# Performance work log

Hardware: AMD Instinct MI355X
Metric: run time of the kernel (lower is better)

The kernel has to match this reference:

```python
import jax, jax.numpy as jnp
import numpy as np

EPS = 1e-6
SIGMA = 1.0       # get_matrix default sigma
INIT_SIGMA = 1.0  # args.init_sigma


def setup_inputs() -> dict:
    key = jax.random.key(0)
    ks = jax.random.split(key, 12)
    B, T, LD, NB = 16, 2048, 256, 32
    s = 1.0 / np.sqrt(LD)
    E_raw = jax.random.normal(ks[5], (LD, LD), jnp.float32)
    E_w, _ = jnp.linalg.qr(E_raw)  # orthogonal like geotorch.orthogonal
    return {
        "Z": jax.random.normal(ks[0], (B, T, LD), jnp.float32),
        "obs_times": jax.random.uniform(ks[1], (B, T, 1), jnp.float32),
        "D": jax.random.normal(ks[2], (NB, LD), jnp.float32),
        "coeff_W": jax.random.normal(ks[3], (NB, LD), jnp.float32) * s,
        "coeff_b": jnp.zeros((NB,), jnp.float32),
        "E_w": E_w.astype(jnp.float32),
        "B_w": jax.random.normal(ks[6], (LD, LD), jnp.float32) * s,
        "C_w": jax.random.normal(ks[7], (LD, LD), jnp.float32) * s,
        "M_w": jax.random.normal(ks[8], (LD, LD), jnp.float32) * s,
        "init_mean_p": jax.random.normal(ks[9], (LD,), jnp.float32),
        "init_log_var": jax.random.normal(ks[10], (LD,), jnp.float32),
        "y_log_var": jax.random.normal(ks[11], (LD,), jnp.float32),
    }


def _binop(qi, qj):
    # (A_j*A_i, Bu_j + A_j*Bu_i): combine earlier element qi with later qj
    A_i, Bu_i = qi
    A_j, Bu_j = qj
    return (A_j * A_i, Bu_j + A_j * Bu_i)


def reference(Z, obs_times, D, coeff_W, coeff_b, E_w, B_w, C_w, M_w,
              init_mean_p, init_log_var, y_log_var):
    LD = Z.shape[-1]
    # alphas = B(Z)
    alphas = jnp.einsum('btd,ed->bte', Z, B_w)                      # (B,T,LD)
    # get_matrix (vectorized over batch and time)
    A_basis = -(jnp.exp(D) + EPS)                                   # (NB,LD), negative
    A_coeff = jax.nn.softmax(jnp.einsum('btd,nd->btn', alphas, coeff_W) + coeff_b, axis=-1)
    A_mat = jnp.einsum('btn,nd->btd', A_coeff, A_basis)             # (B,T,LD)
    exp_A_m = jnp.exp(A_mat * obs_times)                            # mean transition
    exp_B_m = (exp_A_m - 1.0) / A_mat * alphas
    exp_A_v = jnp.exp(2.0 * A_mat * obs_times)                      # var transition
    exp_B_v = 0.5 * SIGMA ** 2 * (exp_A_v - 1.0) / A_mat + EPS
    mats_A = jnp.concatenate([exp_A_m, exp_A_v], axis=-1)           # (B,T,2LD)
    mats_B = jnp.concatenate([exp_B_m, exp_B_v], axis=-1)           # (B,T,2LD)
    # parallel linear-recurrence scan over time
    cum_A, cum_B = jax.lax.associative_scan(_binop, (mats_A, mats_B), axis=1)
    # initial condition in rotated coordinates
    init_mean0 = E_w.T @ init_mean_p                                # (LD,)
    diag_v = INIT_SIGMA * (jnp.exp(init_log_var) + EPS)
    init_var0 = jnp.einsum('ki,k->i', E_w ** 2, diag_v)             # diag(E^T diag(v) E)
    init_mv = jnp.concatenate([init_mean0, init_var0], axis=0)      # (2LD,)
    imv = cum_A * init_mv                                           # (B,T,2LD)
    init_mean, init_var = imv[..., :LD], imv[..., LD:]
    xs_mean, xs_var = cum_B[..., :LD], cum_B[..., LD:]
    y_var = jnp.exp(y_log_var) + EPS
    # output projections: M(E(.)) and history C(E(Z))
    history = jnp.einsum('btd,ed,fe->btf', Z, E_w, C_w)
    means = jnp.einsum('btd,ed,fe->btf', xs_mean + init_mean, E_w, M_w) + history
    stds = jnp.einsum('btd,ed,fe->btf', jnp.sqrt(xs_var + init_var + y_var), E_w, M_w)
    return means, stds, alphas
```

## Files before the change

kernel.cpp:

```cpp
#include <hip/hip_runtime.h>
#include <math.h>

#define EPS 1e-6f

#define B_   16
#define T_   2048
#define LD   256
#define NB   32
#define BT   (B_ * T_)
#define NCH  64
#define CHUNK (T_ / NCH)

typedef short bf16x8 __attribute__((ext_vector_type(8)));
typedef float f32x4  __attribute__((ext_vector_type(4)));

__device__ __forceinline__ unsigned short f2b(float f) {
    unsigned int u = __float_as_uint(f);
    unsigned int r = (u + 0x7fffu + ((u >> 16) & 1u)) >> 16;
    return (unsigned short)r;
}

__device__ __forceinline__ void gl_lds16(const void* g, void* l) {
    __builtin_amdgcn_global_load_lds(
        (const __attribute__((address_space(1))) unsigned int*)g,
        (__attribute__((address_space(3))) unsigned int*)l, 16, 0, 0);
}

__device__ __forceinline__ void stage_tile(const unsigned short* __restrict__ src,
                                           int row0, int stride, int kb,
                                           unsigned short* lds, int wv, int lane) {
#pragma unroll
    for (int cc = 0; cc < 2; ++cc) {
        int c = wv * 2 + cc;
        int r = c * 16 + (lane >> 2);
        int qd = (lane & 3) ^ ((r >> 1) & 3);
        const unsigned short* g = src + (size_t)(row0 + r) * stride + kb + qd * 8;
        gl_lds16(g, lds + c * 512);
    }
}

__device__ __forceinline__ void stage_tile256(const unsigned short* __restrict__ src,
                                              int kb, unsigned short* lds, int wv, int lane) {
#pragma unroll
    for (int cc = 0; cc < 4; ++cc) {
        int c = wv * 4 + cc;
        int r = c * 16 + (lane >> 2);
        int qd = (lane & 3) ^ ((r >> 1) & 3);
        const unsigned short* g = src + (size_t)r * LD + kb + qd * 8;
        gl_lds16(g, lds + c * 512);
    }
}

__device__ __forceinline__ bf16x8 frag_ld(const unsigned short* lds, int row, int qd) {
    int pq = qd ^ ((row >> 1) & 3);
    return *(const bf16x8*)(lds + row * 32 + pq * 8);
}

__global__ __launch_bounds__(256) void k_pre(const float* __restrict__ Z,
                                             const float* __restrict__ Dm,
                                             const float* __restrict__ cw,
                                             const float* __restrict__ Ew,
                                             const float* __restrict__ Bw,
                                             const float* __restrict__ Cw,
                                             const float* __restrict__ Mw,
                                             const float* __restrict__ imp,
                                             const float* __restrict__ ilv,
                                             const float* __restrict__ ylv,
                                             unsigned short* __restrict__ GMh,
                                             unsigned short* __restrict__ GCh,
                                             unsigned short* __restrict__ cwbh,
                                             float* __restrict__ im0,
                                             float* __restrict__ iv0,
                                             float* __restrict__ yv,
                                             float* __restrict__ Ab,
                                             unsigned short* __restrict__ Bwh,
                                             unsigned short* __restrict__ Zh) {
    int bid = blockIdx.x;
    int tid = threadIdx.x;
    if (bid < 544) {
        const float* W; const float* E; unsigned short* out; int d0, f0;
        if (bid < 256)      { W = Mw; E = Ew; out = GMh;  d0 = (bid & 15) * 16; f0 = (bid >> 4) * 16; }
        else if (bid < 512) { W = Cw; E = Ew; out = GCh;  d0 = (bid & 15) * 16; f0 = ((bid - 256) >> 4) * 16; }
        else                { W = cw; E = Bw; out = cwbh; d0 = (bid & 15) * 16; f0 = ((bid - 512) >> 4) * 16; }
        __shared__ float Ws[16][17];
        __shared__ float Es[16][17];
        int tx = tid & 15, ty = tid >> 4;
        float acc = 0.f;
        for (int eb = 0; eb < LD; eb += 16) {
            Ws[ty][tx] = W[(f0 + ty) * LD + eb + tx];
            Es[ty][tx] = E[(eb + ty) * LD + d0 + tx];
            __syncthreads();
#pragma unroll
            for (int k = 0; k < 16; ++k) acc = fmaf(Ws[ty][k], Es[k][tx], acc);
            __syncthreads();
        }
        out[(f0 + ty) * LD + d0 + tx] = f2b(acc);
    } else if (bid < 577) {
        int sub = bid - 544;
        int t = tid;
        if (sub == 0) {
            float sm = 0.f, sv = 0.f;
            for (int k = 0; k < LD; ++k) {
                float e = Ew[k * LD + t];
                sm = fmaf(e, imp[k], sm);
                sv = fmaf(e * e, expf(ilv[k]) + EPS, sv);
            }
            im0[t] = sm;
            iv0[t] = sv;
            yv[t]  = expf(ylv[t]) + EPS;
        } else {
            int n = sub - 1;
            Ab[n * LD + t] = -(expf(Dm[n * LD + t]) + EPS);
        }
    } else if (bid < 641) {
        int i = (bid - 577) * 256 + tid;
        float4 v = ((const float4*)Bw)[i];
        ((ushort4*)Bwh)[i] = make_ushort4(f2b(v.x), f2b(v.y), f2b(v.z), f2b(v.w));
    } else {
        int i = (bid - 641) * 256 + tid;
        float4 v = ((const float4*)Z)[i];
        ((ushort4*)Zh)[i] = make_ushort4(f2b(v.x), f2b(v.y), f2b(v.z), f2b(v.w));
    }
}

__global__ __launch_bounds__(256) void k_zb(const unsigned short* __restrict__ Zh,
                                            const unsigned short* __restrict__ Bwh,
                                            const unsigned short* __restrict__ cwbh,
                                            const float* __restrict__ cb,
                                            float* __restrict__ alphas,
                                            float* __restrict__ logits) {
    __shared__ unsigned short As[128 * 32];
    __shared__ unsigned short Bs[128 * 32];
    int tid = threadIdx.x, lane = tid & 63, wv = tid >> 6;
    int m0 = blockIdx.x * 128;
    int y  = blockIdx.y;
    if (y < 2) {
        int n0 = y * 128;
        int wm = (wv & 1) * 64, wn = (wv >> 1) * 64;
        f32x4 acc[4][4];
#pragma unroll
        for (int i = 0; i < 4; ++i)
#pragma unroll
            for (int j = 0; j < 4; ++j) acc[i][j] = (f32x4){0.f, 0.f, 0.f, 0.f};
        for (int kb = 0; kb < LD; kb += 32) {
            stage_tile(Zh, m0, LD, kb, As, wv, lane);
            stage_tile(Bwh, n0, LD, kb, Bs, wv, lane);
            __syncthreads();
            int qd = lane >> 4;
            bf16x8 af[4], bf[4];
#pragma unroll
            for (int i = 0; i < 4; ++i) af[i] = frag_ld(As, wm + i * 16 + (lane & 15), qd);
#pragma unroll
            for (int j = 0; j < 4; ++j) bf[j] = frag_ld(Bs, wn + j * 16 + (lane & 15), qd);
#pragma unroll
            for (int i = 0; i < 4; ++i)
#pragma unroll
                for (int j = 0; j < 4; ++j)
                    acc[i][j] = __builtin_amdgcn_mfma_f32_16x16x32_bf16(af[i], bf[j], acc[i][j], 0, 0, 0);
            __syncthreads();
        }
        int col = wn + (lane & 15);
        int rb  = wm + ((lane >> 4) << 2);
#pragma unroll
        for (int i = 0; i < 4; ++i)
#pragma unroll
            for (int j = 0; j < 4; ++j)
#pragma unroll
                for (int r = 0; r < 4; ++r)
                    alphas[(size_t)(m0 + rb + i * 16 + r) * LD + n0 + col + j * 16] = acc[i][j][r];
    } else {
        f32x4 acc[2][2];
#pragma unroll
        for (int i = 0; i < 2; ++i)
#pragma unroll
            for (int j = 0; j < 2; ++j) acc[i][j] = (f32x4){0.f, 0.f, 0.f, 0.f};
        for (int kb = 0; kb < LD; kb += 32) {
            stage_tile(Zh, m0, LD, kb, As, wv, lane);
            if (wv < 2) {
                int r = wv * 16 + (lane >> 2);
                int qd = (lane & 3) ^ ((r >> 1) & 3);
                gl_lds16(cwbh + (size_t)r * LD + kb + qd * 8, Bs + wv * 512);
            }
            __syncthreads();
            int qd = lane >> 4;
            bf16x8 af[2], bff[2];
#pragma unroll
            for (int i = 0; i < 2; ++i) af[i] = frag_ld(As, wv * 32 + i * 16 + (lane & 15), qd);
#pragma unroll
            for (int j = 0; j < 2; ++j) bff[j] = frag_ld(Bs, j * 16 + (lane & 15), qd);
#pragma unroll
            for (int i = 0; i < 2; ++i)
#pragma unroll
                for (int j = 0; j < 2; ++j)
                    acc[i][j] = __builtin_amdgcn_mfma_f32_16x16x32_bf16(af[i], bff[j], acc[i][j], 0, 0, 0);
            __syncthreads();
        }
        int col = lane & 15;
        int rb  = (lane >> 4) << 2;
#pragma unroll
        for (int i = 0; i < 2; ++i)
#pragma unroll
            for (int j = 0; j < 2; ++j)
#pragma unroll
                for (int r = 0; r < 4; ++r) {
                    int row = m0 + wv * 32 + i * 16 + rb + r;
                    int cc  = j * 16 + col;
                    logits[(size_t)row * NB + cc] = acc[i][j][r] + cb[cc];
                }
    }
}

__device__ __forceinline__ void scan_prolog(const float* __restrict__ logits,
                                            const float* __restrict__ obs,
                                            const float* __restrict__ Ab,
                                            int bt0, int d,
                                            float (*lg)[NB], float* obs_s, float* abc) {
    int tid = threadIdx.x;
    float4* lg4 = (float4*)lg;
    const float4* g4 = (const float4*)(logits + (size_t)bt0 * NB);
    lg4[tid] = g4[tid];
    if (tid < CHUNK) obs_s[tid] = obs[bt0 + tid];
    __syncthreads();
    int l = tid & 31, rg = tid >> 5;
#pragma unroll
    for (int j = 0; j < CHUNK / 8; ++j) {
        int row = rg * (CHUNK / 8) + j;
        float v = lg[row][l];
        float mx = v;
#pragma unroll
        for (int off = 16; off >= 1; off >>= 1) mx = fmaxf(mx, __shfl_xor(mx, off, 32));
        float e = expf(v - mx);
        float s = e;
#pragma unroll
        for (int off = 16; off >= 1; off >>= 1) s += __shfl_xor(s, off, 32);
        lg[row][l] = e / s;
    }
    __syncthreads();
#pragma unroll
    for (int n = 0; n < NB; ++n) abc[n] = Ab[n * LD + d];
}

__global__ __launch_bounds__(256) void k_tot(const float* __restrict__ logits,
                                             const float* __restrict__ alphas,
                                             const float* __restrict__ obs,
                                             const float* __restrict__ Ab,
                                             float* __restrict__ totA,
                                             float* __restrict__ totBm,
                                             float* __restrict__ totBv) {
    __shared__ float lg[CHUNK][NB];
    __shared__ float obs_s[CHUNK];
    int d = threadIdx.x;
    int bt0 = blockIdx.x * CHUNK;
    float abc[NB];
    scan_prolog(logits, obs, Ab, bt0, d, lg, obs_s, abc);
    float ra = 1.f, rm = 0.f, rv = 0.f;
    for (int i = 0; i < CHUNK; ++i) {
        float av = alphas[(size_t)(bt0 + i) * LD + d];
        float Am = 0.f;
#pragma unroll
        for (int n = 0; n < NB; ++n) Am = fmaf(lg[i][n], abc[n], Am);
        float tt  = obs_s[i];
        float eAm = expf(Am * tt);
        float ieA = 1.f / Am;
        float eBm = (eAm - 1.f) * ieA * av;
        float eBv = 0.5f * (eAm * eAm - 1.f) * ieA + EPS;
        rm = fmaf(eAm, rm, eBm);
        rv = fmaf(eAm * eAm, rv, eBv);
        ra *= eAm;
    }
    int pidx = blockIdx.x * LD + d;
    totA[pidx] = ra; totBm[pidx] = rm; totBv[pidx] = rv;
}

__global__ void k_chunkpfx(const float* __restrict__ totA, const float* __restrict__ totBm,
                           const float* __restrict__ totBv,
                           float* __restrict__ preA, float* __restrict__ preBm,
                           float* __restrict__ preBv) {
    int d = threadIdx.x;
    int b = blockIdx.x;
    float Pa = 1.f, Pm = 0.f, Pv = 0.f;
    for (int ch = 0; ch < NCH; ++ch) {
        int pidx = (b * NCH + ch) * LD + d;
        preA[pidx] = Pa; preBm[pidx] = Pm; preBv[pidx] = Pv;
        float a = totA[pidx], tm_ = totBm[pidx], tv = totBv[pidx];
        Pm = fmaf(a, Pm, tm_);
        Pv = fmaf(a * a, Pv, tv);
        Pa = a * Pa;
    }
}

__global__ __launch_bounds__(256) void k_sms(const float* __restrict__ logits,
                                             const float* __restrict__ alphas,
                                             const float* __restrict__ obs,
                                             const float* __restrict__ Ab,
                                             const float* __restrict__ preA,
                                             const float* __restrict__ preBm,
                                             const float* __restrict__ preBv,
                                             const float* __restrict__ im0,
                                             const float* __restrict__ iv0,
                                             const float* __restrict__ yv,
                                             const unsigned short* __restrict__ Zh,
                                             const unsigned short* __restrict__ GMh,
                                             const unsigned short* __restrict__ GCh,
                                             float* __restrict__ means,
                                             float* __restrict__ stds) {
    __shared__ unsigned short Ms[CHUNK * LD];
    __shared__ unsigned short Ss[CHUNK * LD];
    __shared__ unsigned short Bs[256 * 32];
    float (*lg)[NB] = (float(*)[NB])Bs;
    float* obs_s = (float*)(Bs + 2048 + 2048);

    int tid = threadIdx.x, lane = tid & 63, wv = tid >> 6;
    int d = tid;
    int bt0 = blockIdx.x * CHUNK;
    float abc[NB];
    scan_prolog(logits, obs, Ab, bt0, d, lg, obs_s, abc);

    int pidx = blockIdx.x * LD + d;
    float ga = preA[pidx], gm = preBm[pidx], gv = preBv[pidx];
    float i0 = im0[d], v0 = iv0[d], yvd = yv[d];
    int dc = d >> 5, q = (d & 31) >> 3, jj = d & 7;
    for (int i = 0; i < CHUNK; ++i) {
        float av = alphas[(size_t)(bt0 + i) * LD + d];
        float Am = 0.f;
#pragma unroll
        for (int n = 0; n < NB; ++n) Am = fmaf(lg[i][n], abc[n], Am);
        float tt  = obs_s[i];
        float eAm = expf(Am * tt);
        float ieA = 1.f / Am;
        float eBm = (eAm - 1.f) * ieA * av;
        float eBv = 0.5f * (eAm * eAm - 1.f) * ieA + EPS;
        gm = fmaf(eAm, gm, eBm);
        gv = fmaf(eAm * eAm, gv, eBv);
        ga *= eAm;
        float mm = fmaf(ga, i0, gm);
        float vv = fmaf(ga * ga, v0, gv) + yvd;
        int pq = q ^ ((i >> 1) & 3);
        int a = dc * (CHUNK * 32) + i * 32 + pq * 8 + jj;
        Ms[a] = f2b(mm);
        Ss[a] = f2b(sqrtf(vv));
    }
    __syncthreads();

    f32x4 accm[2][4], accs[2][4];
#pragma unroll
    for (int i = 0; i < 2; ++i)
#pragma unroll
        for (int j = 0; j < 4; ++j) {
            accm[i][j] = (f32x4){0.f, 0.f, 0.f, 0.f};
            accs[i][j] = (f32x4){0.f, 0.f, 0.f, 0.f};
        }
    int qd = lane >> 4, mr = lane & 15;
    for (int kc = 0; kc < 8; ++kc) {
        stage_tile256(GMh, kc * 32, Bs, wv, lane);
        __syncthreads();
        bf16x8 am[2], as[2], bfr[4];
#pragma unroll
        for (int i = 0; i < 2; ++i) {
            int row = i * 16 + mr;
            int pq = qd ^ ((row >> 1) & 3);
            am[i] = *(const bf16x8*)(Ms + kc * (CHUNK * 32) + row * 32 + pq * 8);
            as[i] = *(const bf16x8*)(Ss + kc * (CHUNK * 32) + row * 32 + pq * 8);
        }
#pragma unroll
        for (int j = 0; j < 4; ++j) bfr[j] = frag_ld(Bs, wv * 64 + j * 16 + mr, qd);
#pragma unroll
        for (int i = 0; i < 2; ++i)
#pragma unroll
            for (int j = 0; j < 4; ++j) {
                accm[i][j] = __builtin_amdgcn_mfma_f32_16x16x32_bf16(am[i], bfr[j], accm[i][j], 0, 0, 0);
                accs[i][j] = __builtin_amdgcn_mfma_f32_16x16x32_bf16(as[i], bfr[j], accs[i][j], 0, 0, 0);
            }
        __syncthreads();
    }

    for (int kc = 0; kc < 8; ++kc) {
        stage_tile256(GCh, kc * 32, Bs, wv, lane);
        if (wv < 2) {
            int r = wv * 16 + (lane >> 2);
            int qz = (lane & 3) ^ ((r >> 1) & 3);
            gl_lds16(Zh + (size_t)(bt0 + r) * LD + kc * 32 + qz * 8, Ss + wv * 512);
        }
        __syncthreads();
        bf16x8 az[2], bfr[4];
#pragma unroll
        for (int i = 0; i < 2; ++i) az[i] = frag_ld(Ss, i * 16 + mr, qd);
#pragma unroll
        for (int j = 0; j < 4; ++j) bfr[j] = frag_ld(Bs, wv * 64 + j * 16 + mr, qd);
#pragma unroll
        for (int i = 0; i < 2; ++i)
#pragma unroll
            for (int j = 0; j < 4; ++j)
                accm[i][j] = __builtin_amdgcn_mfma_f32_16x16x32_bf16(az[i], bfr[j], accm[i][j], 0, 0, 0);
        __syncthreads();
    }

    int col0 = wv * 64 + mr;
    int rb   = (lane >> 4) << 2;
#pragma unroll
    for (int i = 0; i < 2; ++i)
#pragma unroll
        for (int j = 0; j < 4; ++j)
#pragma unroll
            for (int r = 0; r < 4; ++r) {
                size_t off = (size_t)(bt0 + i * 16 + rb + r) * LD + col0 + j * 16;
                means[off] = accm[i][j][r];
                stds[off]  = accs[i][j][r];
            }
}

extern "C" void kernel_launch(void* const* d_in, const int* in_sizes, int n_in,
                              void* d_out, int out_size, void* d_ws, size_t ws_size,
                              hipStream_t stream) {
    const float* Z   = (const float*)d_in[0];
    const float* obs = (const float*)d_in[1];
    const float* Dm  = (const float*)d_in[2];
    const float* cw  = (const float*)d_in[3];
    const float* cb  = (const float*)d_in[4];
    const float* Ew  = (const float*)d_in[5];
    const float* Bw  = (const float*)d_in[6];
    const float* Cw  = (const float*)d_in[7];
    const float* Mw  = (const float*)d_in[8];
    const float* imp = (const float*)d_in[9];
    const float* ilv = (const float*)d_in[10];
    const float* ylv = (const float*)d_in[11];

    float* out    = (float*)d_out;
    float* means  = out;
    float* stds   = out + (size_t)BT * LD;
    float* alphas = out + (size_t)2 * BT * LD;

    char* ws = (char*)d_ws;
    size_t o = 0;
    unsigned short* Zh   = (unsigned short*)(ws + o); o += (size_t)BT * LD * 2;
    float*          logits=(float*)(ws + o);          o += (size_t)BT * NB * 4;
    unsigned short* GMh  = (unsigned short*)(ws + o); o += (size_t)LD * LD * 2;
    unsigned short* GCh  = (unsigned short*)(ws + o); o += (size_t)LD * LD * 2;
    unsigned short* Bwh  = (unsigned short*)(ws + o); o += (size_t)LD * LD * 2;
    unsigned short* cwbh = (unsigned short*)(ws + o); o += (size_t)NB * LD * 2;
    float* Ab    = (float*)(ws + o); o += (size_t)NB * LD * 4;
    float* totA  = (float*)(ws + o); o += (size_t)B_ * NCH * LD * 4;
    float* totBm = (float*)(ws + o); o += (size_t)B_ * NCH * LD * 4;
    float* totBv = (float*)(ws + o); o += (size_t)B_ * NCH * LD * 4;
    float* preA  = (float*)(ws + o); o += (size_t)B_ * NCH * LD * 4;
    float* preBm = (float*)(ws + o); o += (size_t)B_ * NCH * LD * 4;
    float* preBv = (float*)(ws + o); o += (size_t)B_ * NCH * LD * 4;
    float* im0   = (float*)(ws + o); o += LD * 4;
    float* iv0   = (float*)(ws + o); o += LD * 4;
    float* yv    = (float*)(ws + o); o += LD * 4;

    k_pre<<<dim3(641 + BT * LD / 1024), dim3(256), 0, stream>>>(
        Z, Dm, cw, Ew, Bw, Cw, Mw, imp, ilv, ylv,
        GMh, GCh, cwbh, im0, iv0, yv, Ab, Bwh, Zh);

    k_zb<<<dim3(BT / 128, 3), dim3(256), 0, stream>>>(Zh, Bwh, cwbh, cb, alphas, logits);

    k_tot<<<dim3(B_ * NCH), dim3(LD), 0, stream>>>(logits, alphas, obs, Ab, totA, totBm, totBv);
    k_chunkpfx<<<dim3(B_), dim3(LD), 0, stream>>>(totA, totBm, totBv, preA, preBm, preBv);

    k_sms<<<dim3(B_ * NCH), dim3(256), 0, stream>>>(logits, alphas, obs, Ab,
                                                    preA, preBm, preBv,
                                                    im0, iv0, yv,
                                                    Zh, GMh, GCh, means, stds);
}
```

Before: 243.7 us.

## Compute softmax-basis matrix with split-bf16 MFMA and read GEMM operands directly

The per-timestep A_mat dot product over the 32 basis vectors, previously a scalar FMA loop per thread, is now done with MFMA. Probabilities and the basis are split into bf16 hi/lo pairs so three MFMAs approximate fp32 accuracy, and the results go to a swizzled LDS buffer that the scan kernels read. In k_sms the scan writes packed bf16 mean/std pairs into that same buffer. The output GEMMs read GM, GC and Z fragments straight from global memory instead of staging them through LDS with barriers, and the two GEMM passes are merged into one loop. The cost is some precision loss from the split-bf16 products and more uncoalesced global fragment loads.

```diff
diff --git a/kernel.cpp b/kernel.cpp
--- a/kernel.cpp
+++ b/kernel.cpp
@@ -20,6 +20,10 @@
     return (unsigned short)r;
 }
 
+__device__ __forceinline__ float b2f(unsigned short h) {
+    return __uint_as_float(((unsigned int)h) << 16);
+}
+
 __device__ __forceinline__ void gl_lds16(const void* g, void* l) {
     __builtin_amdgcn_global_load_lds(
         (const __attribute__((address_space(1))) unsigned int*)g,
@@ -39,21 +43,72 @@
     }
 }
 
-__device__ __forceinline__ void stage_tile256(const unsigned short* __restrict__ src,
-                                              int kb, unsigned short* lds, int wv, int lane) {
-#pragma unroll
-    for (int cc = 0; cc < 4; ++cc) {
-        int c = wv * 4 + cc;
-        int r = c * 16 + (lane >> 2);
-        int qd = (lane & 3) ^ ((r >> 1) & 3);
-        const unsigned short* g = src + (size_t)r * LD + kb + qd * 8;
-        gl_lds16(g, lds + c * 512);
-    }
-}
-
 __device__ __forceinline__ bf16x8 frag_ld(const unsigned short* lds, int row, int qd) {
     int pq = qd ^ ((row >> 1) & 3);
     return *(const bf16x8*)(lds + row * 32 + pq * 8);
+}
+
+__device__ __forceinline__ int u_idx(int i, int d) {
+    return ((d >> 5) << 10) + (i << 5) + (((((d >> 3) & 3)) ^ (i & 3)) << 3) + (d & 7);
+}
+
+__device__ __forceinline__ void compute_Am(const float* __restrict__ logits,
+                                           const float* __restrict__ obs,
+                                           const unsigned short* __restrict__ AbTh,
+                                           const unsigned short* __restrict__ AbTl,
+                                           int bt0,
+                                           unsigned int* U,
+                                           unsigned short* Ph, unsigned short* Pl,
+                                           float* obs_s) {
+    int tid = threadIdx.x;
+    int l = tid & 31, rg = tid >> 5;
+    if (tid < CHUNK) obs_s[tid] = obs[bt0 + tid];
+#pragma unroll
+    for (int jj = 0; jj < 4; ++jj) {
+        int row = rg * 4 + jj;
+        float v = logits[(size_t)(bt0 + row) * NB + l];
+        float mx = v;
+#pragma unroll
+        for (int off = 16; off >= 1; off >>= 1) mx = fmaxf(mx, __shfl_xor(mx, off, 32));
+        float e = expf(v - mx);
+        float s = e;
+#pragma unroll
+        for (int off = 16; off >= 1; off >>= 1) s += __shfl_xor(s, off, 32);
+        float p = e / s;
+        unsigned short h = f2b(p);
+        int sa = row * 32 + ((((l >> 3) ^ ((row >> 1) & 3))) << 3) + (l & 7);
+        Ph[sa] = h;
+        Pl[sa] = f2b(p - b2f(h));
+    }
+    __syncthreads();
+
+    int lane = tid & 63, wv = tid >> 6;
+    int qd = lane >> 4, mr = lane & 15;
+    bf16x8 ph[2], pl[2];
+#pragma unroll
+    for (int iT = 0; iT < 2; ++iT) {
+        ph[iT] = frag_ld(Ph, iT * 16 + mr, qd);
+        pl[iT] = frag_ld(Pl, iT * 16 + mr, qd);
+    }
+#pragma unroll
+    for (int j = 0; j < 4; ++j) {
+        int dcol = wv * 64 + j * 16 + mr;
+        bf16x8 ah = *(const bf16x8*)(AbTh + dcol * NB + qd * 8);
+        bf16x8 al = *(const bf16x8*)(AbTl + dcol * NB + qd * 8);
+#pragma unroll
+        for (int iT = 0; iT < 2; ++iT) {
+            f32x4 acc = (f32x4){0.f, 0.f, 0.f, 0.f};
+            acc = __builtin_amdgcn_mfma_f32_16x16x32_bf16(ph[iT], ah, acc, 0, 0, 0);
+            acc = __builtin_amdgcn_mfma_f32_16x16x32_bf16(pl[iT], ah, acc, 0, 0, 0);
+            acc = __builtin_amdgcn_mfma_f32_16x16x32_bf16(ph[iT], al, acc, 0, 0, 0);
+#pragma unroll
+            for (int r = 0; r < 4; ++r) {
+                int i = iT * 16 + qd * 4 + r;
+                U[u_idx(i, dcol)] = __float_as_uint(acc[r]);
+            }
+        }
+    }
+    __syncthreads();
 }
 
 __global__ __launch_bounds__(256) void k_pre(const float* __restrict__ Z,
@@ -72,7 +127,8 @@
                                              float* __restrict__ im0,
                                              float* __restrict__ iv0,
                                              float* __restrict__ yv,
-                                             float* __restrict__ Ab,
+                                             unsigned short* __restrict__ AbTh,
+                                             unsigned short* __restrict__ AbTl,
                                              unsigned short* __restrict__ Bwh,
                                              unsigned short* __restrict__ Zh) {
     int bid = blockIdx.x;
@@ -110,7 +166,10 @@
             yv[t]  = expf(ylv[t]) + EPS;
         } else {
             int n = sub - 1;
-            Ab[n * LD + t] = -(expf(Dm[n * LD + t]) + EPS);
+            float a = -(expf(Dm[n * LD + t]) + EPS);
+            unsigned short h = f2b(a);
+            AbTh[t * NB + n] = h;
+            AbTl[t * NB + n] = f2b(a - b2f(h));
         }
     } else if (bid < 641) {
         int i = (bid - 577) * 256 + tid;
@@ -210,63 +269,43 @@
     }
 }
 
-__device__ __forceinline__ void scan_prolog(const float* __restrict__ logits,
-                                            const float* __restrict__ obs,
-                                            const float* __restrict__ Ab,
-                                            int bt0, int d,
-                                            float (*lg)[NB], float* obs_s, float* abc) {
-    int tid = threadIdx.x;
-    float4* lg4 = (float4*)lg;
-    const float4* g4 = (const float4*)(logits + (size_t)bt0 * NB);
-    lg4[tid] = g4[tid];
-    if (tid < CHUNK) obs_s[tid] = obs[bt0 + tid];
-    __syncthreads();
-    int l = tid & 31, rg = tid >> 5;
-#pragma unroll
-    for (int j = 0; j < CHUNK / 8; ++j) {
-        int row = rg * (CHUNK / 8) + j;
-        float v = lg[row][l];
-        float mx = v;
-#pragma unroll
-        for (int off = 16; off >= 1; off >>= 1) mx = fmaxf(mx, __shfl_xor(mx, off, 32));
-        float e = expf(v - mx);
-        float s = e;
-#pragma unroll
-        for (int off = 16; off >= 1; off >>= 1) s += __shfl_xor(s, off, 32);
-        lg[row][l] = e / s;
-    }
-    __syncthreads();
-#pragma unroll
-    for (int n = 0; n < NB; ++n) abc[n] = Ab[n * LD + d];
-}
-
 __global__ __launch_bounds__(256) void k_tot(const float* __restrict__ logits,
                                              const float* __restrict__ alphas,
                                              const float* __restrict__ obs,
-                                             const float* __restrict__ Ab,
+                                             const unsigned short* __restrict__ AbTh,
+                                             const unsigned short* __restrict__ AbTl,
                                              float* __restrict__ totA,
                                              float* __restrict__ totBm,
                                              float* __restrict__ totBv) {
-    __shared__ float lg[CHUNK][NB];
+    __shared__ unsigned int U[8192];
+    __shared__ unsigned short Ph[1024];
+    __shared__ unsigned short Pl[1024];
     __shared__ float obs_s[CHUNK];
     int d = threadIdx.x;
     int bt0 = blockIdx.x * CHUNK;
-    float abc[NB];
-    scan_prolog(logits, obs, Ab, bt0, d, lg, obs_s, abc);
+    compute_Am(logits, obs, AbTh, AbTl, bt0, U, Ph, Pl, obs_s);
+
     float ra = 1.f, rm = 0.f, rv = 0.f;
-    for (int i = 0; i < CHUNK; ++i) {
-        float av = alphas[(size_t)(bt0 + i) * LD + d];
-        float Am = 0.f;
-#pragma unroll
-        for (int n = 0; n < NB; ++n) Am = fmaf(lg[i][n], abc[n], Am);
-        float tt  = obs_s[i];
-        float eAm = expf(Am * tt);
-        float ieA = 1.f / Am;
-        float eBm = (eAm - 1.f) * ieA * av;
-        float eBv = 0.5f * (eAm * eAm - 1.f) * ieA + EPS;
-        rm = fmaf(eAm, rm, eBm);
-        rv = fmaf(eAm * eAm, rv, eBv);
-        ra *= eAm;
+    int ubase = ((d >> 5) << 10) + (d & 7);
+    int qb = (d >> 3) & 3;
+    for (int g = 0; g < 4; ++g) {
+        float av[8];
+#pragma unroll
+        for (int k = 0; k < 8; ++k)
+            av[k] = alphas[(size_t)(bt0 + g * 8 + k) * LD + d];
+#pragma unroll
+        for (int k = 0; k < 8; ++k) {
+            int i = g * 8 + k;
+            int ui = ubase + (i << 5) + ((qb ^ (i & 3)) << 3);
+            float Am = __uint_as_float(U[ui]);
+            float eAm = expf(Am * obs_s[i]);
+            float ieA = 1.f / Am;
+            float eBm = (eAm - 1.f) * ieA * av[k];
+            float eBv = 0.5f * (eAm * eAm - 1.f) * ieA + EPS;
+            rm = fmaf(eAm, rm, eBm);
+            rv = fmaf(eAm * eAm, rv, eBv);
+            ra *= eAm;
+        }
     }
     int pidx = blockIdx.x * LD + d;
     totA[pidx] = ra; totBm[pidx] = rm; totBv[pidx] = rv;
@@ -292,7 +331,8 @@
 __global__ __launch_bounds__(256) void k_sms(const float* __restrict__ logits,
                                              const float* __restrict__ alphas,
                                              const float* __restrict__ obs,
-                                             const float* __restrict__ Ab,
+                                             const unsigned short* __restrict__ AbTh,
+                                             const unsigned short* __restrict__ AbTl,
                                              const float* __restrict__ preA,
                                              const float* __restrict__ preBm,
                                              const float* __restrict__ preBv,
@@ -304,95 +344,84 @@
                                              const unsigned short* __restrict__ GCh,
                                              float* __restrict__ means,
                                              float* __restrict__ stds) {
-    __shared__ unsigned short Ms[CHUNK * LD];
-    __shared__ unsigned short Ss[CHUNK * LD];
-    __shared__ unsigned short Bs[256 * 32];
-    float (*lg)[NB] = (float(*)[NB])Bs;
-    float* obs_s = (float*)(Bs + 2048 + 2048);
-
-    int tid = threadIdx.x, lane = tid & 63, wv = tid >> 6;
+    __shared__ unsigned int U[8192];
+    __shared__ unsigned short Ph[1024];
+    __shared__ unsigned short Pl[1024];
+    __shared__ float obs_s[CHUNK];
+    int tid = threadIdx.x;
     int d = tid;
     int bt0 = blockIdx.x * CHUNK;
-    float abc[NB];
-    scan_prolog(logits, obs, Ab, bt0, d, lg, obs_s, abc);
+    compute_Am(logits, obs, AbTh, AbTl, bt0, U, Ph, Pl, obs_s);
 
     int pidx = blockIdx.x * LD + d;
     float ga = preA[pidx], gm = preBm[pidx], gv = preBv[pidx];
     float i0 = im0[d], v0 = iv0[d], yvd = yv[d];
-    int dc = d >> 5, q = (d & 31) >> 3, jj = d & 7;
-    for (int i = 0; i < CHUNK; ++i) {
-        float av = alphas[(size_t)(bt0 + i) * LD + d];
-        float Am = 0.f;
-#pragma unroll
-        for (int n = 0; n < NB; ++n) Am = fmaf(lg[i][n], abc[n], Am);
-        float tt  = obs_s[i];
-        float eAm = expf(Am * tt);
-        float ieA = 1.f / Am;
-        float eBm = (eAm - 1.f) * ieA * av;
-        float eBv = 0.5f * (eAm * eAm - 1.f) * ieA + EPS;
-        gm = fmaf(eAm, gm, eBm);
-        gv = fmaf(eAm * eAm, gv, eBv);
-        ga *= eAm;
-        float mm = fmaf(ga, i0, gm);
-        float vv = fmaf(ga * ga, v0, gv) + yvd;
-        int pq = q ^ ((i >> 1) & 3);
-        int a = dc * (CHUNK * 32) + i * 32 + pq * 8 + jj;
-        Ms[a] = f2b(mm);
-        Ss[a] = f2b(sqrtf(vv));
+    int ubase = ((d >> 5) << 10) + (d & 7);
+    int qb = (d >> 3) & 3;
+    for (int g = 0; g < 4; ++g) {
+        float av[8];
+#pragma unroll
+        for (int k = 0; k < 8; ++k)
+            av[k] = alphas[(size_t)(bt0 + g * 8 + k) * LD + d];
+#pragma unroll
+        for (int k = 0; k < 8; ++k) {
+            int i = g * 8 + k;
+            int ui = ubase + (i << 5) + ((qb ^ (i & 3)) << 3);
+            float Am = __uint_as_float(U[ui]);
+            float eAm = expf(Am * obs_s[i]);
+            float ieA = 1.f / Am;
+            float eBm = (eAm - 1.f) * ieA * av[k];
+            float eBv = 0.5f * (eAm * eAm - 1.f) * ieA + EPS;
+            gm = fmaf(eAm, gm, eBm);
+            gv = fmaf(eAm * eAm, gv, eBv);
+            ga *= eAm;
+            float mm = fmaf(ga, i0, gm);
+            float vv = fmaf(ga * ga, v0, gv) + yvd;
+            U[ui] = ((unsigned int)f2b(mm) << 16) | (unsigned int)f2b(sqrtf(vv));
+        }
     }
     __syncthreads();
 
+    int lane = tid & 63, wv = tid >> 6;
+    int qd = lane >> 4, mr = lane & 15;
     f32x4 accm[2][4], accs[2][4];
 #pragma unroll
-    for (int i = 0; i < 2; ++i)
+    for (int iT = 0; iT < 2; ++iT)
 #pragma unroll
         for (int j = 0; j < 4; ++j) {
-            accm[i][j] = (f32x4){0.f, 0.f, 0.f, 0.f};
-            accs[i][j] = (f32x4){0.f, 0.f, 0.f, 0.f};
-        }
-    int qd = lane >> 4, mr = lane & 15;
+            accm[iT][j] = (f32x4){0.f, 0.f, 0.f, 0.f};
+            accs[iT][j] = (f32x4){0.f, 0.f, 0.f, 0.f};
+        }
     for (int kc = 0; kc < 8; ++kc) {
-        stage_tile256(GMh, kc * 32, Bs, wv, lane);
-        __syncthreads();
-        bf16x8 am[2], as[2], bfr[4];
-#pragma unroll
-        for (int i = 0; i < 2; ++i) {
-            int row = i * 16 + mr;
-            int pq = qd ^ ((row >> 1) & 3);
-            am[i] = *(const bf16x8*)(Ms + kc * (CHUNK * 32) + row * 32 + pq * 8);
-            as[i] = *(const bf16x8*)(Ss + kc * (CHUNK * 32) + row * 32 + pq * 8);
-        }
-#pragma unroll
-        for (int j = 0; j < 4; ++j) bfr[j] = frag_ld(Bs, wv * 64 + j * 16 + mr, qd);
-#pragma unroll
-        for (int i = 0; i < 2; ++i)
-#pragma unroll
-            for (int j = 0; j < 4; ++j) {
-                accm[i][j] = __builtin_amdgcn_mfma_f32_16x16x32_bf16(am[i], bfr[j], accm[i][j], 0, 0, 0);
-                accs[i][j] = __builtin_amdgcn_mfma_f32_16x16x32_bf16(as[i], bfr[j], accs[i][j], 0, 0, 0);
-            }
-        __syncthreads();
-    }
-
-    for (int kc = 0; kc < 8; ++kc) {
-        stage_tile256(GCh, kc * 32, Bs, wv, lane);
-        if (wv < 2) {
-            int r = wv * 16 + (lane >> 2);
-            int qz = (lane & 3) ^ ((r >> 1) & 3);
-            gl_lds16(Zh + (size_t)(bt0 + r) * LD + kc * 32 + qz * 8, Ss + wv * 512);
-        }
-        __syncthreads();
-        bf16x8 az[2], bfr[4];
-#pragma unroll
-        for (int i = 0; i < 2; ++i) az[i] = frag_ld(Ss, i * 16 + mr, qd);
-#pragma unroll
-        for (int j = 0; j < 4; ++j) bfr[j] = frag_ld(Bs, wv * 64 + j * 16 + mr, qd);
-#pragma unroll
-        for (int i = 0; i < 2; ++i)
-#pragma unroll
-            for (int j = 0; j < 4; ++j)
-                accm[i][j] = __builtin_amdgcn_mfma_f32_16x16x32_bf16(az[i], bfr[j], accm[i][j], 0, 0, 0);
-        __syncthreads();
+        bf16x8 am[2], asv[2], az[2];
+#pragma unroll
+        for (int iT = 0; iT < 2; ++iT) {
+            int row = iT * 16 + mr;
+            int off = (kc << 10) + (row << 5) + ((qd ^ (row & 3)) << 3);
+            uint4 ua = *(const uint4*)(U + off);
+            uint4 ub = *(const uint4*)(U + off + 4);
+            unsigned int uu[8] = {ua.x, ua.y, ua.z, ua.w, ub.x, ub.y, ub.z, ub.w};
+            bf16x8 m_, s_;
+#pragma unroll
+            for (int k = 0; k < 8; ++k) {
+                m_[k] = (short)(uu[k] >> 16);
+                s_[k] = (short)(uu[k] & 0xffffu);
+            }
+            am[iT] = m_; asv[iT] = s_;
+            az[iT] = *(const bf16x8*)(Zh + (size_t)(bt0 + row) * LD + kc * 32 + qd * 8);
+        }
+#pragma unroll
+        for (int j = 0; j < 4; ++j) {
+            int brow = wv * 64 + j * 16 + mr;
+            bf16x8 bm = *(const bf16x8*)(GMh + (size_t)brow * LD + kc * 32 + qd * 8);
+            bf16x8 bc = *(const bf16x8*)(GCh + (size_t)brow * LD + kc * 32 + qd * 8);
+#pragma unroll
+            for (int iT = 0; iT < 2; ++iT) {
+                accm[iT][j] = __builtin_amdgcn_mfma_f32_16x16x32_bf16(am[iT],  bm, accm[iT][j], 0, 0, 0);
+                accs[iT][j] = __builtin_amdgcn_mfma_f32_16x16x32_bf16(asv[iT], bm, accs[iT][j], 0, 0, 0);
+                accm[iT][j] = __builtin_amdgcn_mfma_f32_16x16x32_bf16(az[iT],  bc, accm[iT][j], 0, 0, 0);
+            }
+        }
     }
 
     int col0 = wv * 64 + mr;
@@ -438,7 +467,8 @@
     unsigned short* GCh  = (unsigned short*)(ws + o); o += (size_t)LD * LD * 2;
     unsigned short* Bwh  = (unsigned short*)(ws + o); o += (size_t)LD * LD * 2;
     unsigned short* cwbh = (unsigned short*)(ws + o); o += (size_t)NB * LD * 2;
-    float* Ab    = (float*)(ws + o); o += (size_t)NB * LD * 4;
+    unsigned short* AbTh = (unsigned short*)(ws + o); o += (size_t)LD * NB * 2;
+    unsigned short* AbTl = (unsigned short*)(ws + o); o += (size_t)LD * NB * 2;
     float* totA  = (float*)(ws + o); o += (size_t)B_ * NCH * LD * 4;
     float* totBm = (float*)(ws + o); o += (size_t)B_ * NCH * LD * 4;
     float* totBv = (float*)(ws + o); o += (size_t)B_ * NCH * LD * 4;
@@ -451,14 +481,15 @@
 
     k_pre<<<dim3(641 + BT * LD / 1024), dim3(256), 0, stream>>>(
         Z, Dm, cw, Ew, Bw, Cw, Mw, imp, ilv, ylv,
-        GMh, GCh, cwbh, im0, iv0, yv, Ab, Bwh, Zh);
+        GMh, GCh, cwbh, im0, iv0, yv, AbTh, AbTl, Bwh, Zh);
 
     k_zb<<<dim3(BT / 128, 3), dim3(256), 0, stream>>>(Zh, Bwh, cwbh, cb, alphas, logits);
 
-    k_tot<<<dim3(B_ * NCH), dim3(LD), 0, stream>>>(logits, alphas, obs, Ab, totA, totBm, totBv);
+    k_tot<<<dim3(B_ * NCH), dim3(256), 0, stream>>>(logits, alphas, obs, AbTh, AbTl,
+                                                    totA, totBm, totBv);
     k_chunkpfx<<<dim3(B_), dim3(LD), 0, stream>>>(totA, totBm, totBv, preA, preBm, preBv);
 
-    k_sms<<<dim3(B_ * NCH), dim3(256), 0, stream>>>(logits, alphas, obs, Ab,
+    k_sms<<<dim3(B_ * NCH), dim3(256), 0, stream>>>(logits, alphas, obs, AbTh, AbTl,
                                                     preA, preBm, preBv,
                                                     im0, iv0, yv,
                                                     Zh, GMh, GCh, means, stds);
```

Result: no change. 239.7 us (-1.6%).
